# Optimization experiments

Measured on AMD Instinct MI355X. Metric: run time of the kernel, lower is better.

## Reference

```python
import jax, jax.numpy as jnp
import numpy as np

WS = (8, 8)          # window_size
HEADS = 8
DH = 64              # dim_head
SHIFT = (4, 4)
SCALE = DH ** -0.5


def setup_inputs() -> dict:
    key = jax.random.key(0)
    ks = jax.random.split(key, 5)
    dim = 64
    inner = HEADS * DH  # 512
    b, h, w = 4, 192, 192
    x = jax.random.normal(ks[0], (b, h, w, dim), dtype=jnp.float32)
    Wq = jax.random.normal(ks[1], (dim, inner), dtype=jnp.float32) * (dim ** -0.5)
    Wkv = jax.random.normal(ks[2], (dim, 2 * inner), dtype=jnp.float32) * (dim ** -0.5)
    Wo = jax.random.normal(ks[3], (inner, dim), dtype=jnp.float32) * (inner ** -0.5)
    bo = jnp.zeros((dim,), dtype=jnp.float32)
    seq_l = WS[0] * WS[1]
    pos_emb = jax.random.normal(ks[4], (1, HEADS, seq_l, seq_l), dtype=jnp.float32)
    return {"x": x, "Wq": Wq, "Wkv": Wkv, "Wo": Wo, "bo": bo, "pos_emb": pos_emb}


def reference(x, Wq, Wkv, Wo, bo, pos_emb):
    b, h, w, c = x.shape
    L = WS[0] * WS[1]  # 64 tokens per window
    if SHIFT[0] > 0:
        x = jnp.roll(x, shift=(-SHIFT[0], -SHIFT[1]), axis=(1, 2))
    # NOTE: original uses a raw .view() here (row-major reshape), NOT an 8x8
    # window partition. Replicate exactly.
    nw = b * (h // WS[0]) * (w // WS[1])
    x_inp = x.reshape(nw, L, c)                      # [nw, 64, c]
    q = x_inp @ Wq                                   # [nw, 64, inner]
    kv = x_inp @ Wkv
    k, v = jnp.split(kv, 2, axis=-1)
    # original: raw view (nw, L, inner) -> (nw, heads, L, dh) (not a transpose)
    q = q.reshape(nw, HEADS, L, DH) * SCALE
    k = k.reshape(nw, HEADS, L, DH)
    v = v.reshape(nw, HEADS, L, DH)
    sim = jnp.einsum('bhid,bhjd->bhij', q, k) + pos_emb
    attn = jax.nn.softmax(sim, axis=-1)
    out = jnp.einsum('bhij,bhjd->bhid', attn, v)     # [nw, heads, 64, dh]
    # original: raw view back to (nw, L, inner)
    out = out.reshape(nw, L, HEADS * DH)
    out = out @ Wo + bo                              # [nw, 64, c]
    out = out.reshape(b, h, w, c)
    if SHIFT[0] > 0:
        out = jnp.roll(out, shift=(SHIFT[0], SHIFT[1]), axis=(1, 2))
    return out
```

## Files before the change

### kernel.cpp

```cpp
#include <hip/hip_runtime.h>
#include <stdint.h>

typedef __attribute__((ext_vector_type(8))) short bf16x8;
typedef __attribute__((ext_vector_type(4))) short s16x4;
typedef __attribute__((ext_vector_type(4))) float f32x4;

#define THREADS 256
constexpr int NWIN = 2304;

constexpr int WCATT_E = 0;
constexpr int WOT_E   = 98304;
constexpr int POS_E   = 131072;
constexpr size_t WS_NEED = 327680;

__device__ __forceinline__ short f2bf(float f) {
  uint32_t u = __builtin_bit_cast(uint32_t, f);
  u += 0x7fffu + ((u >> 16) & 1u);
  return (short)(u >> 16);
}
__device__ __forceinline__ float bf2f(short s) {
  uint32_t u = ((uint32_t)(uint16_t)s) << 16;
  return __builtin_bit_cast(float, u);
}
__device__ __forceinline__ int swz(int row, int h) {
  return ((((row ^ (row >> 2) ^ (row >> 3)) & 7) ^ h) << 4);
}

__global__ void wmsa_prep(const float* __restrict__ Wq, const float* __restrict__ Wkv,
                          const float* __restrict__ Wo, const float* __restrict__ pos,
                          short* __restrict__ ws) {
  int idx = blockIdx.x * 256 + threadIdx.x;
  if (idx < 32768) {
    int n = idx & 511, k = idx >> 9;
    ws[WCATT_E + n * 64 + k] = f2bf(Wq[k * 512 + n] * 0.125f);
  } else if (idx < 98304) {
    int j = idx - 32768;
    int nkv = j & 1023, k = j >> 10;
    ws[WCATT_E + (512 + nkv) * 64 + k] = f2bf(Wkv[k * 1024 + nkv]);
  } else if (idx < 131072) {
    int j = idx - 98304;
    int n = j & 63, k = j >> 6;
    ws[WOT_E + n * 512 + k] = f2bf(Wo[k * 64 + n]);
  } else if (idx < 163840) {
    int j = idx - 131072;
    ws[POS_E + j] = f2bf(pos[j]);
  }
}

__global__ __launch_bounds__(512, 2)
void wmsa_mfma4(const float* __restrict__ x, const float* __restrict__ bo,
                const short* __restrict__ ws, float* __restrict__ out) {
  extern __shared__ __align__(16) char lds[];
  const int tid = threadIdx.x;
  const int wv = tid >> 6;
  const int l  = tid & 63;
  const int lr = l & 15;
  const int lg = l >> 4;

  const int bid = blockIdx.x;
  const int q   = bid >> 2;
  const int hp  = bid & 3;

  bf16x8 xa[4][2];
  #pragma unroll
  for (int win = 0; win < 4; ++win) {
    int w   = 4 * q + win;
    int bb  = w / 576;
    int rem = (w * 64) % 36864;
    int hh  = rem / 192;
    int ww0 = rem % 192;
    int src_h = (hh + 4) % 192;
    const float* xp = x + (size_t)(bb * 192 + src_h) * 12288;
    int tok = 16 * hp + lr;
    int sw = ww0 + tok + 4; if (sw >= 192) sw -= 192;
    const float* xq = xp + sw * 64;
    #pragma unroll
    for (int ks = 0; ks < 2; ++ks) {
      float4 a = *(const float4*)(xq + ks * 32 + lg * 8);
      float4 b = *(const float4*)(xq + ks * 32 + lg * 8 + 4);
      bf16x8 v;
      v[0] = f2bf(a.x); v[1] = f2bf(a.y); v[2] = f2bf(a.z); v[3] = f2bf(a.w);
      v[4] = f2bf(b.x); v[5] = f2bf(b.y); v[6] = f2bf(b.z); v[7] = f2bf(b.w);
      xa[win][ks] = v;
    }
  }

  #pragma unroll
  for (int t = 0; t < 8; ++t) {
    int nt = wv + 8 * t;
    int nload = nt * 16 + lr;
    bf16x8 b0 = *(const bf16x8*)(ws + WCATT_E + nload * 64 + lg * 8);
    bf16x8 b1 = *(const bf16x8*)(ws + WCATT_E + nload * 64 + 32 + lg * 8);
    const bool isQ = (t < 4);
    int i  = (lr & 7) * 8 + ((nt >> 2) & 7);
    int h2 = lr >> 3;
    int d0 = (nt & 3) * 16 + lg * 4;
    int off = (isQ ? 0 : 16384) + h2 * 8192 + i * 128 + ((d0 * 2) ^ swz(i, h2));
    #pragma unroll
    for (int win = 0; win < 4; ++win) {
      f32x4 acc = {0.f, 0.f, 0.f, 0.f};
      acc = __builtin_amdgcn_mfma_f32_16x16x32_bf16(b0, xa[win][0], acc, 0, 0, 0);
      acc = __builtin_amdgcn_mfma_f32_16x16x32_bf16(b1, xa[win][1], acc, 0, 0, 0);
      s16x4 pk;
      #pragma unroll
      for (int r = 0; r < 4; ++r) pk[r] = f2bf(acc[r]);
      *(s16x4*)(lds + win * 32768 + off) = pk;
    }
  }

  const int bq = wv & 3, aq = wv >> 2;
  f32x4 vacc[4][4];
  #pragma unroll
  for (int u = 0; u < 4; ++u) {
    int ntile = (aq * 4 + u) * 4 + bq;
    int nload = (64 + ntile) * 16 + lr;
    bf16x8 b0 = *(const bf16x8*)(ws + WCATT_E + nload * 64 + lg * 8);
    bf16x8 b1 = *(const bf16x8*)(ws + WCATT_E + nload * 64 + 32 + lg * 8);
    #pragma unroll
    for (int win = 0; win < 4; ++win) {
      f32x4 acc = {0.f, 0.f, 0.f, 0.f};
      acc = __builtin_amdgcn_mfma_f32_16x16x32_bf16(xa[win][0], b0, acc, 0, 0, 0);
      acc = __builtin_amdgcn_mfma_f32_16x16x32_bf16(xa[win][1], b1, acc, 0, 0, 0);
      vacc[win][u] = acc;
    }
  }
  __syncthreads();

  const int hl = (wv >> 1) & 1;
  const int ih = wv & 1;
  const int hglob = 2 * hp + hl;
  const int wbase = aq;

  s16x4 posr[2][4];
  #pragma unroll
  for (int it = 0; it < 2; ++it) {
    int i = (ih * 2 + it) * 16 + lr;
    const short* pp = ws + POS_E + hglob * 4096 + i * 64;
    #pragma unroll
    for (int jt = 0; jt < 4; ++jt)
      posr[it][jt] = *(const s16x4*)(pp + jt * 16 + lg * 4);
  }

  #pragma unroll
  for (int c = 0; c < 2; ++c) {
    char* ldw = lds + (wbase + 2 * c) * 32768;
    f32x4 s[2][4];
    #pragma unroll
    for (int it = 0; it < 2; ++it)
      #pragma unroll
      for (int jt = 0; jt < 4; ++jt) s[it][jt] = (f32x4){0.f, 0.f, 0.f, 0.f};

    #pragma unroll
    for (int ks = 0; ks < 2; ++ks) {
      bf16x8 kb[4], qa[2];
      #pragma unroll
      for (int jt = 0; jt < 4; ++jt) {
        int j = jt * 16 + lr;
        kb[jt] = *(const bf16x8*)(ldw + 16384 + hl * 8192 + j * 128 + ((ks * 64 + lg * 16) ^ swz(j, hl)));
      }
      #pragma unroll
      for (int it = 0; it < 2; ++it) {
        int i = (ih * 2 + it) * 16 + lr;
        qa[it] = *(const bf16x8*)(ldw + hl * 8192 + i * 128 + ((ks * 64 + lg * 16) ^ swz(i, hl)));
      }
      __builtin_amdgcn_s_setprio(1);
      #pragma unroll
      for (int it = 0; it < 2; ++it)
        #pragma unroll
        for (int jt = 0; jt < 4; ++jt)
          s[it][jt] = __builtin_amdgcn_mfma_f32_16x16x32_bf16(kb[jt], qa[it], s[it][jt], 0, 0, 0);
      __builtin_amdgcn_s_setprio(0);
    }

    #pragma unroll
    for (int it = 0; it < 2; ++it) {
      int i = (ih * 2 + it) * 16 + lr;
      float sum = 0.f;
      #pragma unroll
      for (int jt = 0; jt < 4; ++jt)
        #pragma unroll
        for (int r = 0; r < 4; ++r) {
          float pv = __expf(s[it][jt][r] + bf2f(posr[it][jt][r]));
          s[it][jt][r] = pv;
          sum += pv;
        }
      sum += __shfl_xor(sum, 16);
      sum += __shfl_xor(sum, 32);
      float rinv = 1.f / sum;
      #pragma unroll
      for (int jt = 0; jt < 4; ++jt) {
        s16x4 pk;
        #pragma unroll
        for (int r = 0; r < 4; ++r) pk[r] = f2bf(s[it][jt][r] * rinv);
        *(s16x4*)(ldw + hl * 8192 + i * 128 + ((jt * 32 + lg * 8) ^ swz(i, hl))) = pk;
      }
    }
  }
  __syncthreads();

  {
    int d = bq * 16 + lr;
    #pragma unroll
    for (int win = 0; win < 4; ++win)
      #pragma unroll
      for (int r = 0; r < 4; ++r) {
        int tl = lg * 4 + r;
        int h2 = tl >> 3;
        int jb = (tl & 7) * 16 + aq * 8;
        s16x4 pk;
        #pragma unroll
        for (int u = 0; u < 4; ++u) pk[u] = f2bf(vacc[win][u][r]);
        *(s16x4*)(lds + win * 32768 + 16384 + h2 * 8192 + d * 128 + (jb ^ swz(d, h2))) = pk;
      }
  }
  __syncthreads();

  bf16x8 wofr[16];
  #pragma unroll
  for (int ks = 0; ks < 16; ++ks)
    wofr[ks] = *(const bf16x8*)(ws + WOT_E + (bq * 16 + lr) * 512 + ks * 32 + lg * 8);

  #pragma unroll
  for (int c = 0; c < 2; ++c) {
    char* ldw = lds + (wbase + 2 * c) * 32768;
    f32x4 o[2][4];
    #pragma unroll
    for (int it = 0; it < 2; ++it)
      #pragma unroll
      for (int dt = 0; dt < 4; ++dt) o[it][dt] = (f32x4){0.f, 0.f, 0.f, 0.f};
    #pragma unroll
    for (int ks = 0; ks < 2; ++ks) {
      bf16x8 vb[4], pa[2];
      #pragma unroll
      for (int dt = 0; dt < 4; ++dt) {
        int d = dt * 16 + lr;
        vb[dt] = *(const bf16x8*)(ldw + 16384 + hl * 8192 + d * 128 + ((ks * 64 + lg * 16) ^ swz(d, hl)));
      }
      #pragma unroll
      for (int it = 0; it < 2; ++it) {
        int i = (ih * 2 + it) * 16 + lr;
        pa[it] = *(const bf16x8*)(ldw + hl * 8192 + i * 128 + ((ks * 64 + lg * 16) ^ swz(i, hl)));
      }
      __builtin_amdgcn_s_setprio(1);
      #pragma unroll
      for (int it = 0; it < 2; ++it)
        #pragma unroll
        for (int dt = 0; dt < 4; ++dt)
          o[it][dt] = __builtin_amdgcn_mfma_f32_16x16x32_bf16(vb[dt], pa[it], o[it][dt], 0, 0, 0);
      __builtin_amdgcn_s_setprio(0);
    }
    #pragma unroll
    for (int it = 0; it < 2; ++it) {
      int i  = (ih * 2 + it) * 16 + lr;
      int lm = 8 * hl + (i >> 3);
      int rp = lm * 8 + (i & 7);
      #pragma unroll
      for (int dt = 0; dt < 4; ++dt) {
        s16x4 pk;
        #pragma unroll
        for (int r = 0; r < 4; ++r) pk[r] = f2bf(o[it][dt][r]);
        *(s16x4*)(ldw + rp * 128 + ((dt * 32 + lg * 8) ^ swz(rp, 0))) = pk;
      }
    }
  }
  __syncthreads();

  f32x4 oacc0 = {0.f, 0.f, 0.f, 0.f};
  f32x4 oacc1 = {0.f, 0.f, 0.f, 0.f};
  #pragma unroll
  for (int ks = 0; ks < 16; ++ks) {
    int rp = lr * 8 + (ks >> 1);
    int boff = rp * 128 + (((ks & 1) * 64 + lg * 16) ^ swz(rp, 0));
    bf16x8 bA = *(const bf16x8*)(lds + wbase * 32768 + boff);
    bf16x8 bB = *(const bf16x8*)(lds + (wbase + 2) * 32768 + boff);
    oacc0 = __builtin_amdgcn_mfma_f32_16x16x32_bf16(wofr[ks], bA, oacc0, 0, 0, 0);
    oacc1 = __builtin_amdgcn_mfma_f32_16x16x32_bf16(wofr[ks], bB, oacc1, 0, 0, 0);
  }
  {
    int c0 = bq * 16 + lg * 4;
    float4 bo4 = *(const float4*)(bo + c0);
    int tok = 16 * hp + lr;
    #pragma unroll
    for (int c = 0; c < 2; ++c) {
      int w   = 4 * q + wbase + 2 * c;
      int bb  = w / 576;
      int rem = (w * 64) % 36864;
      int hh  = rem / 192;
      int ww0 = rem % 192;
      int src_h = (hh + 4) % 192;
      float* orow = out + (size_t)(bb * 192 + src_h) * 12288;
      int sw = ww0 + tok + 4; if (sw >= 192) sw -= 192;
      f32x4 oa = c ? oacc1 : oacc0;
      float4 ov;
      ov.x = oa[0] + bo4.x; ov.y = oa[1] + bo4.y;
      ov.z = oa[2] + bo4.z; ov.w = oa[3] + bo4.w;
      *(float4*)(orow + sw * 64 + c0) = ov;
    }
  }
}

__global__ __launch_bounds__(THREADS, 2)
void wmsa_mfma(const float* __restrict__ x, const float* __restrict__ bo,
               const short* __restrict__ ws, float* __restrict__ out) {
  __shared__ __align__(16) char lds[65536];
  const int tid = threadIdx.x;
  const int wv = tid >> 6;
  const int l  = tid & 63;
  const int lr = l & 15;
  const int lg = l >> 4;

  const int bid = blockIdx.x;
  const int p   = bid >> 2;
  const int hp  = bid & 3;

  const float* xrow[2];
  float* orow[2];
  int ww0a[2];
  #pragma unroll
  for (int win = 0; win < 2; ++win) {
    int w   = 2 * p + win;
    int t0  = w * 64;
    int bb  = t0 / 36864;
    int rem = t0 % 36864;
    int hh  = rem / 192;
    ww0a[win] = rem % 192;
    int src_h = (hh + 4) % 192;
    xrow[win] = x + (size_t)(bb * 192 + src_h) * 12288;
    orow[win] = out + (size_t)(bb * 192 + src_h) * 12288;
  }

  bf16x8 xa[2][2];
  #pragma unroll
  for (int win = 0; win < 2; ++win) {
    int tok = 16 * hp + lr;
    int sw = ww0a[win] + tok + 4; if (sw >= 192) sw -= 192;
    const float* xp = xrow[win] + sw * 64;
    #pragma unroll
    for (int ks = 0; ks < 2; ++ks) {
      float4 a = *(const float4*)(xp + ks * 32 + lg * 8);
      float4 b = *(const float4*)(xp + ks * 32 + lg * 8 + 4);
      bf16x8 v;
      v[0] = f2bf(a.x); v[1] = f2bf(a.y); v[2] = f2bf(a.z); v[3] = f2bf(a.w);
      v[4] = f2bf(b.x); v[5] = f2bf(b.y); v[6] = f2bf(b.z); v[7] = f2bf(b.w);
      xa[win][ks] = v;
    }
  }

  #pragma unroll 4
  for (int t = 0; t < 16; ++t) {
    int nt = wv + 4 * t;
    int nload = nt * 16 + lr;
    bf16x8 b0 = *(const bf16x8*)(ws + WCATT_E + nload * 64 + lg * 8);
    bf16x8 b1 = *(const bf16x8*)(ws + WCATT_E + nload * 64 + 32 + lg * 8);
    const bool isQ = (t < 8);
    int i  = (lr & 7) * 8 + (t & 7);
    int h2 = lr >> 3;
    int d0 = wv * 16 + lg * 4;
    int off = (isQ ? 0 : 16384) + h2 * 8192 + i * 128 + ((d0 * 2) ^ swz(i, h2));
    #pragma unroll
    for (int win = 0; win < 2; ++win) {
      f32x4 acc = {0.f, 0.f, 0.f, 0.f};
      acc = __builtin_amdgcn_mfma_f32_16x16x32_bf16(b0, xa[win][0], acc, 0, 0, 0);
      acc = __builtin_amdgcn_mfma_f32_16x16x32_bf16(b1, xa[win][1], acc, 0, 0, 0);
      s16x4 pk;
      #pragma unroll
      for (int r = 0; r < 4; ++r) pk[r] = f2bf(acc[r]);
      *(s16x4*)(lds + win * 32768 + off) = pk;
    }
  }

  f32x4 vacc[2][8];
  #pragma unroll
  for (int tv = 0; tv < 8; ++tv) {
    int nload = (64 + wv + 4 * tv) * 16 + lr;
    bf16x8 b0 = *(const bf16x8*)(ws + WCATT_E + nload * 64 + lg * 8);
    bf16x8 b1 = *(const bf16x8*)(ws + WCATT_E + nload * 64 + 32 + lg * 8);
    #pragma unroll
    for (int win = 0; win < 2; ++win) {
      f32x4 acc = {0.f, 0.f, 0.f, 0.f};
      acc = __builtin_amdgcn_mfma_f32_16x16x32_bf16(xa[win][0], b0, acc, 0, 0, 0);
      acc = __builtin_amdgcn_mfma_f32_16x16x32_bf16(xa[win][1], b1, acc, 0, 0, 0);
      vacc[win][tv] = acc;
    }
  }
  __syncthreads();

  const int hl = wv >> 1;
  const int ih = wv & 1;
  const int hglob = 2 * hp + hl;

  s16x4 posr[2][4];
  #pragma unroll
  for (int it = 0; it < 2; ++it) {
    int i = (ih * 2 + it) * 16 + lr;
    const short* pp = ws + POS_E + hglob * 4096 + i * 64;
    #pragma unroll
    for (int jt = 0; jt < 4; ++jt)
      posr[it][jt] = *(const s16x4*)(pp + jt * 16 + lg * 4);
  }

  #pragma unroll
  for (int win = 0; win < 2; ++win) {
    char* ldw = lds + win * 32768;
    f32x4 s[2][4];
    #pragma unroll
    for (int it = 0; it < 2; ++it)
      #pragma unroll
      for (int jt = 0; jt < 4; ++jt) s[it][jt] = (f32x4){0.f, 0.f, 0.f, 0.f};

    #pragma unroll
    for (int ks = 0; ks < 2; ++ks) {
      bf16x8 kb[4], qa[2];
      #pragma unroll
      for (int jt = 0; jt < 4; ++jt) {
        int j = jt * 16 + lr;
        kb[jt] = *(const bf16x8*)(ldw + 16384 + hl * 8192 + j * 128 + ((ks * 64 + lg * 16) ^ swz(j, hl)));
      }
      #pragma unroll
      for (int it = 0; it < 2; ++it) {
        int i = (ih * 2 + it) * 16 + lr;
        qa[it] = *(const bf16x8*)(ldw + hl * 8192 + i * 128 + ((ks * 64 + lg * 16) ^ swz(i, hl)));
      }
      __builtin_amdgcn_s_setprio(1);
      #pragma unroll
      for (int it = 0; it < 2; ++it)
        #pragma unroll
        for (int jt = 0; jt < 4; ++jt)
          s[it][jt] = __builtin_amdgcn_mfma_f32_16x16x32_bf16(kb[jt], qa[it], s[it][jt], 0, 0, 0);
      __builtin_amdgcn_s_setprio(0);
    }

    #pragma unroll
    for (int it = 0; it < 2; ++it) {
      int i = (ih * 2 + it) * 16 + lr;
      float sum = 0.f;
      #pragma unroll
      for (int jt = 0; jt < 4; ++jt)
        #pragma unroll
        for (int r = 0; r < 4; ++r) {
          float pv = __expf(s[it][jt][r] + bf2f(posr[it][jt][r]));
          s[it][jt][r] = pv;
          sum += pv;
        }
      sum += __shfl_xor(sum, 16);
      sum += __shfl_xor(sum, 32);
      float rinv = 1.f / sum;
      #pragma unroll
      for (int jt = 0; jt < 4; ++jt) {
        s16x4 pk;
        #pragma unroll
        for (int r = 0; r < 4; ++r) pk[r] = f2bf(s[it][jt][r] * rinv);
        *(s16x4*)(ldw + hl * 8192 + i * 128 + ((jt * 32 + lg * 8) ^ swz(i, hl))) = pk;
      }
    }
  }
  __syncthreads();

  {
    int d = wv * 16 + lr;
    #pragma unroll
    for (int win = 0; win < 2; ++win)
      #pragma unroll
      for (int r = 0; r < 4; ++r) {
        int tl = lg * 4 + r;
        int h2 = tl >> 3;
        int slot = tl & 7;
        bf16x8 pk;
        #pragma unroll
        for (int tv = 0; tv < 8; ++tv) pk[tv] = f2bf(vacc[win][tv][r]);
        *(bf16x8*)(lds + win * 32768 + 16384 + h2 * 8192 + d * 128 + ((slot * 16) ^ swz(d, h2))) = pk;
      }
  }
  __syncthreads();

  bf16x8 wofr[16];
  #pragma unroll
  for (int ks = 0; ks < 16; ++ks)
    wofr[ks] = *(const bf16x8*)(ws + WOT_E + (wv * 16 + lr) * 512 + ks * 32 + lg * 8);

  #pragma unroll
  for (int win = 0; win < 2; ++win) {
    char* ldw = lds + win * 32768;
    f32x4 o[2][4];
    #pragma unroll
    for (int it = 0; it < 2; ++it)
      #pragma unroll
      for (int dt = 0; dt < 4; ++dt) o[it][dt] = (f32x4){0.f, 0.f, 0.f, 0.f};
    #pragma unroll
    for (int ks = 0; ks < 2; ++ks) {
      bf16x8 vb[4], pa[2];
      #pragma unroll
      for (int dt = 0; dt < 4; ++dt) {
        int d = dt * 16 + lr;
        vb[dt] = *(const bf16x8*)(ldw + 16384 + hl * 8192 + d * 128 + ((ks * 64 + lg * 16) ^ swz(d, hl)));
      }
      #pragma unroll
      for (int it = 0; it < 2; ++it) {
        int i = (ih * 2 + it) * 16 + lr;
        pa[it] = *(const bf16x8*)(ldw + hl * 8192 + i * 128 + ((ks * 64 + lg * 16) ^ swz(i, hl)));
      }
      __builtin_amdgcn_s_setprio(1);
      #pragma unroll
      for (int it = 0; it < 2; ++it)
        #pragma unroll
        for (int dt = 0; dt < 4; ++dt)
          o[it][dt] = __builtin_amdgcn_mfma_f32_16x16x32_bf16(vb[dt], pa[it], o[it][dt], 0, 0, 0);
      __builtin_amdgcn_s_setprio(0);
    }
    #pragma unroll
    for (int it = 0; it < 2; ++it) {
      int i  = (ih * 2 + it) * 16 + lr;
      int lm = 8 * hl + (i >> 3);
      int rp = lm * 8 + (i & 7);
      #pragma unroll
      for (int dt = 0; dt < 4; ++dt) {
        s16x4 pk;
        #pragma unroll
        for (int r = 0; r < 4; ++r) pk[r] = f2bf(o[it][dt][r]);
        *(s16x4*)(ldw + rp * 128 + ((dt * 32 + lg * 8) ^ swz(rp, 0))) = pk;
      }
    }
  }
  __syncthreads();

  f32x4 oacc[2];
  oacc[0] = (f32x4){0.f, 0.f, 0.f, 0.f};
  oacc[1] = (f32x4){0.f, 0.f, 0.f, 0.f};
  #pragma unroll
  for (int ks = 0; ks < 16; ++ks) {
    int rp = lr * 8 + (ks >> 1);
    int boff = rp * 128 + (((ks & 1) * 64 + lg * 16) ^ swz(rp, 0));
    #pragma unroll
    for (int win = 0; win < 2; ++win) {
      bf16x8 bfrOH = *(const bf16x8*)(lds + win * 32768 + boff);
      oacc[win] = __builtin_amdgcn_mfma_f32_16x16x32_bf16(wofr[ks], bfrOH, oacc[win], 0, 0, 0);
    }
  }
  {
    int c0 = wv * 16 + lg * 4;
    float4 bo4 = *(const float4*)(bo + c0);
    int tok = 16 * hp + lr;
    #pragma unroll
    for (int win = 0; win < 2; ++win) {
      int sw = ww0a[win] + tok + 4; if (sw >= 192) sw -= 192;
      float4 ov;
      ov.x = oacc[win][0] + bo4.x; ov.y = oacc[win][1] + bo4.y;
      ov.z = oacc[win][2] + bo4.z; ov.w = oacc[win][3] + bo4.w;
      *(float4*)(orow[win] + sw * 64 + c0) = ov;
    }
  }
}

extern "C" void kernel_launch(void* const* d_in, const int* in_sizes, int n_in,
                              void* d_out, int out_size, void* d_ws, size_t ws_size,
                              hipStream_t stream) {
  const float* x    = (const float*)d_in[0];
  const float* Wq   = (const float*)d_in[1];
  const float* Wkv  = (const float*)d_in[2];
  const float* Wo   = (const float*)d_in[3];
  const float* bo   = (const float*)d_in[4];
  const float* pos  = (const float*)d_in[5];
  float* o = (float*)d_out;
  if (ws_size >= WS_NEED) {
    wmsa_prep<<<dim3(640), dim3(256), 0, stream>>>(Wq, Wkv, Wo, pos, (short*)d_ws);
    hipError_t e = hipFuncSetAttribute((const void*)wmsa_mfma4,
                                       hipFuncAttributeMaxDynamicSharedMemorySize, 131072);
    if (e == hipSuccess) {
      wmsa_mfma4<<<dim3(NWIN), dim3(512), 131072, stream>>>(x, bo, (const short*)d_ws, o);
    } else {
      wmsa_mfma<<<dim3(NWIN * 2), dim3(THREADS), 0, stream>>>(x, bo, (const short*)d_ws, o);
    }
  } else {
    wmsa_prep<<<dim3(640), dim3(256), 0, stream>>>(Wq, Wkv, Wo, pos, (short*)d_ws);
    wmsa_mfma<<<dim3(NWIN * 2), dim3(THREADS), 0, stream>>>(x, bo, (const short*)d_ws, o);
  }
}
```

Baseline: 179.8 us.

## Add 3-window 768-thread kernel with wave-specialized Q/K and V projection

Adds a new fused kernel in which each block handles three windows with 12 waves. Eight waves compute the Q/K projections while four compute V and write it transposed into LDS, which removes the separate V transpose pass and one barrier. After that, each group of four waves runs attention for one window. It uses 144 KB of dynamic LDS, which allows only one block per CU, and it falls back to the 4-window kernel if that LDS size cannot be set. The older 256-thread fallback kernel is removed.

```diff
diff --git a/kernel.cpp b/kernel.cpp
--- a/kernel.cpp
+++ b/kernel.cpp
@@ -47,6 +47,247 @@
   }
 }
 
+__global__ __launch_bounds__(768, 3)
+void wmsa_mfma3(const float* __restrict__ x, const float* __restrict__ bo,
+                const short* __restrict__ ws, float* __restrict__ out) {
+  extern __shared__ __align__(16) char lds[];
+  const int tid = threadIdx.x;
+  const int wv = tid >> 6;
+  const int l  = tid & 63;
+  const int lr = l & 15;
+  const int lg = l >> 4;
+
+  const int bid  = blockIdx.x;
+  const int trip = bid >> 2;
+  const int hp   = bid & 3;
+
+  bf16x8 xa[3][2];
+  #pragma unroll
+  for (int win = 0; win < 3; ++win) {
+    int w   = 3 * trip + win;
+    int bb  = w / 576;
+    int rem = (w % 576) * 64;
+    int hh  = rem / 192;
+    int ww0 = rem % 192;
+    int src_h = (hh + 4) % 192;
+    const float* xp = x + (size_t)(bb * 192 + src_h) * 12288;
+    int tok = 16 * hp + lr;
+    int sw = ww0 + tok + 4; if (sw >= 192) sw -= 192;
+    const float* xq = xp + sw * 64;
+    #pragma unroll
+    for (int ks = 0; ks < 2; ++ks) {
+      float4 a = *(const float4*)(xq + ks * 32 + lg * 8);
+      float4 b = *(const float4*)(xq + ks * 32 + lg * 8 + 4);
+      bf16x8 v;
+      v[0] = f2bf(a.x); v[1] = f2bf(a.y); v[2] = f2bf(a.z); v[3] = f2bf(a.w);
+      v[4] = f2bf(b.x); v[5] = f2bf(b.y); v[6] = f2bf(b.z); v[7] = f2bf(b.w);
+      xa[win][ks] = v;
+    }
+  }
+
+  const int sect = wv >> 2;
+  const int sl   = wv & 3;
+  if (sect < 2) {
+    const int base = sect * 16384;
+    #pragma unroll
+    for (int t = 0; t < 8; ++t) {
+      int ntl = sl + 4 * t;
+      int nload = (sect * 32 + ntl) * 16 + lr;
+      bf16x8 b0 = *(const bf16x8*)(ws + WCATT_E + nload * 64 + lg * 8);
+      bf16x8 b1 = *(const bf16x8*)(ws + WCATT_E + nload * 64 + 32 + lg * 8);
+      int i  = (lr & 7) * 8 + t;
+      int h2 = lr >> 3;
+      int d0 = sl * 16 + lg * 4;
+      int off = base + h2 * 8192 + i * 128 + ((d0 * 2) ^ swz(i, h2));
+      #pragma unroll
+      for (int win = 0; win < 3; ++win) {
+        f32x4 acc = {0.f, 0.f, 0.f, 0.f};
+        acc = __builtin_amdgcn_mfma_f32_16x16x32_bf16(b0, xa[win][0], acc, 0, 0, 0);
+        acc = __builtin_amdgcn_mfma_f32_16x16x32_bf16(b1, xa[win][1], acc, 0, 0, 0);
+        s16x4 pk;
+        #pragma unroll
+        for (int r = 0; r < 4; ++r) pk[r] = f2bf(acc[r]);
+        *(s16x4*)(lds + win * 49152 + off) = pk;
+      }
+    }
+  } else {
+    #pragma unroll
+    for (int g = 0; g < 2; ++g) {
+      f32x4 vg[3][4];
+      #pragma unroll
+      for (int u = 0; u < 4; ++u) {
+        int ntile = (g * 4 + u) * 4 + sl;
+        int nload = (64 + ntile) * 16 + lr;
+        bf16x8 b0 = *(const bf16x8*)(ws + WCATT_E + nload * 64 + lg * 8);
+        bf16x8 b1 = *(const bf16x8*)(ws + WCATT_E + nload * 64 + 32 + lg * 8);
+        #pragma unroll
+        for (int win = 0; win < 3; ++win) {
+          f32x4 acc = {0.f, 0.f, 0.f, 0.f};
+          acc = __builtin_amdgcn_mfma_f32_16x16x32_bf16(xa[win][0], b0, acc, 0, 0, 0);
+          acc = __builtin_amdgcn_mfma_f32_16x16x32_bf16(xa[win][1], b1, acc, 0, 0, 0);
+          vg[win][u] = acc;
+        }
+      }
+      int d = sl * 16 + lr;
+      #pragma unroll
+      for (int win = 0; win < 3; ++win)
+        #pragma unroll
+        for (int r = 0; r < 4; ++r) {
+          int tl = lg * 4 + r;
+          int h2 = tl >> 3;
+          int jb = (tl & 7) * 16 + g * 8;
+          s16x4 pk;
+          #pragma unroll
+          for (int u = 0; u < 4; ++u) pk[u] = f2bf(vg[win][u][r]);
+          *(s16x4*)(lds + win * 49152 + 32768 + h2 * 8192 + d * 128 + (jb ^ swz(d, h2))) = pk;
+        }
+    }
+  }
+  __syncthreads();
+
+  const int awin = wv >> 2;
+  const int hl   = (wv >> 1) & 1;
+  const int ih   = wv & 1;
+  const int hglob = 2 * hp + hl;
+  char* ldw = lds + awin * 49152;
+
+  s16x4 posr[2][4];
+  #pragma unroll
+  for (int it = 0; it < 2; ++it) {
+    int i = (ih * 2 + it) * 16 + lr;
+    const short* pp = ws + POS_E + hglob * 4096 + i * 64;
+    #pragma unroll
+    for (int jt = 0; jt < 4; ++jt)
+      posr[it][jt] = *(const s16x4*)(pp + jt * 16 + lg * 4);
+  }
+
+  f32x4 s[2][4];
+  #pragma unroll
+  for (int it = 0; it < 2; ++it)
+    #pragma unroll
+    for (int jt = 0; jt < 4; ++jt) s[it][jt] = (f32x4){0.f, 0.f, 0.f, 0.f};
+
+  #pragma unroll
+  for (int ks = 0; ks < 2; ++ks) {
+    bf16x8 kb[4], qa[2];
+    #pragma unroll
+    for (int jt = 0; jt < 4; ++jt) {
+      int j = jt * 16 + lr;
+      kb[jt] = *(const bf16x8*)(ldw + 16384 + hl * 8192 + j * 128 + ((ks * 64 + lg * 16) ^ swz(j, hl)));
+    }
+    #pragma unroll
+    for (int it = 0; it < 2; ++it) {
+      int i = (ih * 2 + it) * 16 + lr;
+      qa[it] = *(const bf16x8*)(ldw + hl * 8192 + i * 128 + ((ks * 64 + lg * 16) ^ swz(i, hl)));
+    }
+    __builtin_amdgcn_s_setprio(1);
+    #pragma unroll
+    for (int it = 0; it < 2; ++it)
+      #pragma unroll
+      for (int jt = 0; jt < 4; ++jt)
+        s[it][jt] = __builtin_amdgcn_mfma_f32_16x16x32_bf16(kb[jt], qa[it], s[it][jt], 0, 0, 0);
+    __builtin_amdgcn_s_setprio(0);
+  }
+
+  #pragma unroll
+  for (int it = 0; it < 2; ++it) {
+    int i = (ih * 2 + it) * 16 + lr;
+    float sum = 0.f;
+    #pragma unroll
+    for (int jt = 0; jt < 4; ++jt)
+      #pragma unroll
+      for (int r = 0; r < 4; ++r) {
+        float pv = __expf(s[it][jt][r] + bf2f(posr[it][jt][r]));
+        s[it][jt][r] = pv;
+        sum += pv;
+      }
+    sum += __shfl_xor(sum, 16);
+    sum += __shfl_xor(sum, 32);
+    float rinv = 1.f / sum;
+    #pragma unroll
+    for (int jt = 0; jt < 4; ++jt) {
+      s16x4 pk;
+      #pragma unroll
+      for (int r = 0; r < 4; ++r) pk[r] = f2bf(s[it][jt][r] * rinv);
+      *(s16x4*)(ldw + hl * 8192 + i * 128 + ((jt * 32 + lg * 8) ^ swz(i, hl))) = pk;
+    }
+  }
+
+  const int ct = wv & 3;
+  bf16x8 wofr[16];
+  #pragma unroll
+  for (int ks = 0; ks < 16; ++ks)
+    wofr[ks] = *(const bf16x8*)(ws + WOT_E + (ct * 16 + lr) * 512 + ks * 32 + lg * 8);
+
+  f32x4 o[2][4];
+  #pragma unroll
+  for (int it = 0; it < 2; ++it)
+    #pragma unroll
+    for (int dt = 0; dt < 4; ++dt) o[it][dt] = (f32x4){0.f, 0.f, 0.f, 0.f};
+  #pragma unroll
+  for (int ks = 0; ks < 2; ++ks) {
+    bf16x8 vb[4], pa[2];
+    #pragma unroll
+    for (int dt = 0; dt < 4; ++dt) {
+      int d = dt * 16 + lr;
+      vb[dt] = *(const bf16x8*)(ldw + 32768 + hl * 8192 + d * 128 + ((ks * 64 + lg * 16) ^ swz(d, hl)));
+    }
+    #pragma unroll
+    for (int it = 0; it < 2; ++it) {
+      int i = (ih * 2 + it) * 16 + lr;
+      pa[it] = *(const bf16x8*)(ldw + hl * 8192 + i * 128 + ((ks * 64 + lg * 16) ^ swz(i, hl)));
+    }
+    __builtin_amdgcn_s_setprio(1);
+    #pragma unroll
+    for (int it = 0; it < 2; ++it)
+      #pragma unroll
+      for (int dt = 0; dt < 4; ++dt)
+        o[it][dt] = __builtin_amdgcn_mfma_f32_16x16x32_bf16(vb[dt], pa[it], o[it][dt], 0, 0, 0);
+    __builtin_amdgcn_s_setprio(0);
+  }
+
+  #pragma unroll
+  for (int it = 0; it < 2; ++it) {
+    int i  = (ih * 2 + it) * 16 + lr;
+    int lm = 8 * hl + (i >> 3);
+    int rp = lm * 8 + (i & 7);
+    #pragma unroll
+    for (int dt = 0; dt < 4; ++dt) {
+      s16x4 pk;
+      #pragma unroll
+      for (int r = 0; r < 4; ++r) pk[r] = f2bf(o[it][dt][r]);
+      *(s16x4*)(ldw + rp * 128 + ((dt * 32 + lg * 8) ^ swz(rp, 0))) = pk;
+    }
+  }
+  __syncthreads();
+
+  f32x4 oacc = {0.f, 0.f, 0.f, 0.f};
+  #pragma unroll
+  for (int ks = 0; ks < 16; ++ks) {
+    int rp = lr * 8 + (ks >> 1);
+    int boff = rp * 128 + (((ks & 1) * 64 + lg * 16) ^ swz(rp, 0));
+    bf16x8 bfrOH = *(const bf16x8*)(lds + awin * 49152 + boff);
+    oacc = __builtin_amdgcn_mfma_f32_16x16x32_bf16(wofr[ks], bfrOH, oacc, 0, 0, 0);
+  }
+  {
+    int c0 = ct * 16 + lg * 4;
+    float4 bo4 = *(const float4*)(bo + c0);
+    int w   = 3 * trip + awin;
+    int bb  = w / 576;
+    int rem = (w % 576) * 64;
+    int hh  = rem / 192;
+    int ww0 = rem % 192;
+    int src_h = (hh + 4) % 192;
+    float* orow = out + (size_t)(bb * 192 + src_h) * 12288;
+    int tok = 16 * hp + lr;
+    int sw = ww0 + tok + 4; if (sw >= 192) sw -= 192;
+    float4 ov;
+    ov.x = oacc[0] + bo4.x; ov.y = oacc[1] + bo4.y;
+    ov.z = oacc[2] + bo4.z; ov.w = oacc[3] + bo4.w;
+    *(float4*)(orow + sw * 64 + c0) = ov;
+  }
+}
+
 __global__ __launch_bounds__(512, 2)
 void wmsa_mfma4(const float* __restrict__ x, const float* __restrict__ bo,
                 const short* __restrict__ ws, float* __restrict__ out) {
@@ -299,258 +540,6 @@
   }
 }
 
-__global__ __launch_bounds__(THREADS, 2)
-void wmsa_mfma(const float* __restrict__ x, const float* __restrict__ bo,
-               const short* __restrict__ ws, float* __restrict__ out) {
-  __shared__ __align__(16) char lds[65536];
-  const int tid = threadIdx.x;
-  const int wv = tid >> 6;
-  const int l  = tid & 63;
-  const int lr = l & 15;
-  const int lg = l >> 4;
-
-  const int bid = blockIdx.x;
-  const int p   = bid >> 2;
-  const int hp  = bid & 3;
-
-  const float* xrow[2];
-  float* orow[2];
-  int ww0a[2];
-  #pragma unroll
-  for (int win = 0; win < 2; ++win) {
-    int w   = 2 * p + win;
-    int t0  = w * 64;
-    int bb  = t0 / 36864;
-    int rem = t0 % 36864;
-    int hh  = rem / 192;
-    ww0a[win] = rem % 192;
-    int src_h = (hh + 4) % 192;
-    xrow[win] = x + (size_t)(bb * 192 + src_h) * 12288;
-    orow[win] = out + (size_t)(bb * 192 + src_h) * 12288;
-  }
-
-  bf16x8 xa[2][2];
-  #pragma unroll
-  for (int win = 0; win < 2; ++win) {
-    int tok = 16 * hp + lr;
-    int sw = ww0a[win] + tok + 4; if (sw >= 192) sw -= 192;
-    const float* xp = xrow[win] + sw * 64;
-    #pragma unroll
-    for (int ks = 0; ks < 2; ++ks) {
-      float4 a = *(const float4*)(xp + ks * 32 + lg * 8);
-      float4 b = *(const float4*)(xp + ks * 32 + lg * 8 + 4);
-      bf16x8 v;
-      v[0] = f2bf(a.x); v[1] = f2bf(a.y); v[2] = f2bf(a.z); v[3] = f2bf(a.w);
-      v[4] = f2bf(b.x); v[5] = f2bf(b.y); v[6] = f2bf(b.z); v[7] = f2bf(b.w);
-      xa[win][ks] = v;
-    }
-  }
-
-  #pragma unroll 4
-  for (int t = 0; t < 16; ++t) {
-    int nt = wv + 4 * t;
-    int nload = nt * 16 + lr;
-    bf16x8 b0 = *(const bf16x8*)(ws + WCATT_E + nload * 64 + lg * 8);
-    bf16x8 b1 = *(const bf16x8*)(ws + WCATT_E + nload * 64 + 32 + lg * 8);
-    const bool isQ = (t < 8);
-    int i  = (lr & 7) * 8 + (t & 7);
-    int h2 = lr >> 3;
-    int d0 = wv * 16 + lg * 4;
-    int off = (isQ ? 0 : 16384) + h2 * 8192 + i * 128 + ((d0 * 2) ^ swz(i, h2));
-    #pragma unroll
-    for (int win = 0; win < 2; ++win) {
-      f32x4 acc = {0.f, 0.f, 0.f, 0.f};
-      acc = __builtin_amdgcn_mfma_f32_16x16x32_bf16(b0, xa[win][0], acc, 0, 0, 0);
-      acc = __builtin_amdgcn_mfma_f32_16x16x32_bf16(b1, xa[win][1], acc, 0, 0, 0);
-      s16x4 pk;
-      #pragma unroll
-      for (int r = 0; r < 4; ++r) pk[r] = f2bf(acc[r]);
-      *(s16x4*)(lds + win * 32768 + off) = pk;
-    }
-  }
-
-  f32x4 vacc[2][8];
-  #pragma unroll
-  for (int tv = 0; tv < 8; ++tv) {
-    int nload = (64 + wv + 4 * tv) * 16 + lr;
-    bf16x8 b0 = *(const bf16x8*)(ws + WCATT_E + nload * 64 + lg * 8);
-    bf16x8 b1 = *(const bf16x8*)(ws + WCATT_E + nload * 64 + 32 + lg * 8);
-    #pragma unroll
-    for (int win = 0; win < 2; ++win) {
-      f32x4 acc = {0.f, 0.f, 0.f, 0.f};
-      acc = __builtin_amdgcn_mfma_f32_16x16x32_bf16(xa[win][0], b0, acc, 0, 0, 0);
-      acc = __builtin_amdgcn_mfma_f32_16x16x32_bf16(xa[win][1], b1, acc, 0, 0, 0);
-      vacc[win][tv] = acc;
-    }
-  }
-  __syncthreads();
-
-  const int hl = wv >> 1;
-  const int ih = wv & 1;
-  const int hglob = 2 * hp + hl;
-
-  s16x4 posr[2][4];
-  #pragma unroll
-  for (int it = 0; it < 2; ++it) {
-    int i = (ih * 2 + it) * 16 + lr;
-    const short* pp = ws + POS_E + hglob * 4096 + i * 64;
-    #pragma unroll
-    for (int jt = 0; jt < 4; ++jt)
-      posr[it][jt] = *(const s16x4*)(pp + jt * 16 + lg * 4);
-  }
-
-  #pragma unroll
-  for (int win = 0; win < 2; ++win) {
-    char* ldw = lds + win * 32768;
-    f32x4 s[2][4];
-    #pragma unroll
-    for (int it = 0; it < 2; ++it)
-      #pragma unroll
-      for (int jt = 0; jt < 4; ++jt) s[it][jt] = (f32x4){0.f, 0.f, 0.f, 0.f};
-
-    #pragma unroll
-    for (int ks = 0; ks < 2; ++ks) {
-      bf16x8 kb[4], qa[2];
-      #pragma unroll
-      for (int jt = 0; jt < 4; ++jt) {
-        int j = jt * 16 + lr;
-        kb[jt] = *(const bf16x8*)(ldw + 16384 + hl * 8192 + j * 128 + ((ks * 64 + lg * 16) ^ swz(j, hl)));
-      }
-      #pragma unroll
-      for (int it = 0; it < 2; ++it) {
-        int i = (ih * 2 + it) * 16 + lr;
-        qa[it] = *(const bf16x8*)(ldw + hl * 8192 + i * 128 + ((ks * 64 + lg * 16) ^ swz(i, hl)));
-      }
-      __builtin_amdgcn_s_setprio(1);
-      #pragma unroll
-      for (int it = 0; it < 2; ++it)
-        #pragma unroll
-        for (int jt = 0; jt < 4; ++jt)
-          s[it][jt] = __builtin_amdgcn_mfma_f32_16x16x32_bf16(kb[jt], qa[it], s[it][jt], 0, 0, 0);
-      __builtin_amdgcn_s_setprio(0);
-    }
-
-    #pragma unroll
-    for (int it = 0; it < 2; ++it) {
-      int i = (ih * 2 + it) * 16 + lr;
-      float sum = 0.f;
-      #pragma unroll
-      for (int jt = 0; jt < 4; ++jt)
-        #pragma unroll
-        for (int r = 0; r < 4; ++r) {
-          float pv = __expf(s[it][jt][r] + bf2f(posr[it][jt][r]));
-          s[it][jt][r] = pv;
-          sum += pv;
-        }
-      sum += __shfl_xor(sum, 16);
-      sum += __shfl_xor(sum, 32);
-      float rinv = 1.f / sum;
-      #pragma unroll
-      for (int jt = 0; jt < 4; ++jt) {
-        s16x4 pk;
-        #pragma unroll
-        for (int r = 0; r < 4; ++r) pk[r] = f2bf(s[it][jt][r] * rinv);
-        *(s16x4*)(ldw + hl * 8192 + i * 128 + ((jt * 32 + lg * 8) ^ swz(i, hl))) = pk;
-      }
-    }
-  }
-  __syncthreads();
-
-  {
-    int d = wv * 16 + lr;
-    #pragma unroll
-    for (int win = 0; win < 2; ++win)
-      #pragma unroll
-      for (int r = 0; r < 4; ++r) {
-        int tl = lg * 4 + r;
-        int h2 = tl >> 3;
-        int slot = tl & 7;
-        bf16x8 pk;
-        #pragma unroll
-        for (int tv = 0; tv < 8; ++tv) pk[tv] = f2bf(vacc[win][tv][r]);
-        *(bf16x8*)(lds + win * 32768 + 16384 + h2 * 8192 + d * 128 + ((slot * 16) ^ swz(d, h2))) = pk;
-      }
-  }
-  __syncthreads();
-
-  bf16x8 wofr[16];
-  #pragma unroll
-  for (int ks = 0; ks < 16; ++ks)
-    wofr[ks] = *(const bf16x8*)(ws + WOT_E + (wv * 16 + lr) * 512 + ks * 32 + lg * 8);
-
-  #pragma unroll
-  for (int win = 0; win < 2; ++win) {
-    char* ldw = lds + win * 32768;
-    f32x4 o[2][4];
-    #pragma unroll
-    for (int it = 0; it < 2; ++it)
-      #pragma unroll
-      for (int dt = 0; dt < 4; ++dt) o[it][dt] = (f32x4){0.f, 0.f, 0.f, 0.f};
-    #pragma unroll
-    for (int ks = 0; ks < 2; ++ks) {
-      bf16x8 vb[4], pa[2];
-      #pragma unroll
-      for (int dt = 0; dt < 4; ++dt) {
-        int d = dt * 16 + lr;
-        vb[dt] = *(const bf16x8*)(ldw + 16384 + hl * 8192 + d * 128 + ((ks * 64 + lg * 16) ^ swz(d, hl)));
-      }
-      #pragma unroll
-      for (int it = 0; it < 2; ++it) {
-        int i = (ih * 2 + it) * 16 + lr;
-        pa[it] = *(const bf16x8*)(ldw + hl * 8192 + i * 128 + ((ks * 64 + lg * 16) ^ swz(i, hl)));
-      }
-      __builtin_amdgcn_s_setprio(1);
-      #pragma unroll
-      for (int it = 0; it < 2; ++it)
-        #pragma unroll
-        for (int dt = 0; dt < 4; ++dt)
-          o[it][dt] = __builtin_amdgcn_mfma_f32_16x16x32_bf16(vb[dt], pa[it], o[it][dt], 0, 0, 0);
-      __builtin_amdgcn_s_setprio(0);
-    }
-    #pragma unroll
-    for (int it = 0; it < 2; ++it) {
-      int i  = (ih * 2 + it) * 16 + lr;
-      int lm = 8 * hl + (i >> 3);
-      int rp = lm * 8 + (i & 7);
-      #pragma unroll
-      for (int dt = 0; dt < 4; ++dt) {
-        s16x4 pk;
-        #pragma unroll
-        for (int r = 0; r < 4; ++r) pk[r] = f2bf(o[it][dt][r]);
-        *(s16x4*)(ldw + rp * 128 + ((dt * 32 + lg * 8) ^ swz(rp, 0))) = pk;
-      }
-    }
-  }
-  __syncthreads();
-
-  f32x4 oacc[2];
-  oacc[0] = (f32x4){0.f, 0.f, 0.f, 0.f};
-  oacc[1] = (f32x4){0.f, 0.f, 0.f, 0.f};
-  #pragma unroll
-  for (int ks = 0; ks < 16; ++ks) {
-    int rp = lr * 8 + (ks >> 1);
-    int boff = rp * 128 + (((ks & 1) * 64 + lg * 16) ^ swz(rp, 0));
-    #pragma unroll
-    for (int win = 0; win < 2; ++win) {
-      bf16x8 bfrOH = *(const bf16x8*)(lds + win * 32768 + boff);
-      oacc[win] = __builtin_amdgcn_mfma_f32_16x16x32_bf16(wofr[ks], bfrOH, oacc[win], 0, 0, 0);
-    }
-  }
-  {
-    int c0 = wv * 16 + lg * 4;
-    float4 bo4 = *(const float4*)(bo + c0);
-    int tok = 16 * hp + lr;
-    #pragma unroll
-    for (int win = 0; win < 2; ++win) {
-      int sw = ww0a[win] + tok + 4; if (sw >= 192) sw -= 192;
-      float4 ov;
-      ov.x = oacc[win][0] + bo4.x; ov.y = oacc[win][1] + bo4.y;
-      ov.z = oacc[win][2] + bo4.z; ov.w = oacc[win][3] + bo4.w;
-      *(float4*)(orow[win] + sw * 64 + c0) = ov;
-    }
-  }
-}
-
 extern "C" void kernel_launch(void* const* d_in, const int* in_sizes, int n_in,
                               void* d_out, int out_size, void* d_ws, size_t ws_size,
                               hipStream_t stream) {
@@ -561,17 +550,15 @@
   const float* bo   = (const float*)d_in[4];
   const float* pos  = (const float*)d_in[5];
   float* o = (float*)d_out;
-  if (ws_size >= WS_NEED) {
-    wmsa_prep<<<dim3(640), dim3(256), 0, stream>>>(Wq, Wkv, Wo, pos, (short*)d_ws);
-    hipError_t e = hipFuncSetAttribute((const void*)wmsa_mfma4,
-                                       hipFuncAttributeMaxDynamicSharedMemorySize, 131072);
-    if (e == hipSuccess) {
-      wmsa_mfma4<<<dim3(NWIN), dim3(512), 131072, stream>>>(x, bo, (const short*)d_ws, o);
-    } else {
-      wmsa_mfma<<<dim3(NWIN * 2), dim3(THREADS), 0, stream>>>(x, bo, (const short*)d_ws, o);
-    }
+  wmsa_prep<<<dim3(640), dim3(256), 0, stream>>>(Wq, Wkv, Wo, pos, (short*)d_ws);
+  hipError_t e3 = hipFuncSetAttribute((const void*)wmsa_mfma3,
+                                      hipFuncAttributeMaxDynamicSharedMemorySize, 147456);
+  if (e3 == hipSuccess) {
+    wmsa_mfma3<<<dim3(NWIN / 3 * 4), dim3(768), 147456, stream>>>(x, bo, (const short*)d_ws, o);
   } else {
-    wmsa_prep<<<dim3(640), dim3(256), 0, stream>>>(Wq, Wkv, Wo, pos, (short*)d_ws);
-    wmsa_mfma<<<dim3(NWIN * 2), dim3(THREADS), 0, stream>>>(x, bo, (const short*)d_ws, o);
-  }
-}
+    hipError_t e4 = hipFuncSetAttribute((const void*)wmsa_mfma4,
+                                        hipFuncAttributeMaxDynamicSharedMemorySize, 131072);
+    (void)e4;
+    wmsa_mfma4<<<dim3(NWIN), dim3(512), 131072, stream>>>(x, bo, (const short*)d_ws, o);
+  }
+}
```

After: 238.2 us. +32.4%, slower.
